# Optimization experiments

Measured on AMD Instinct MI355X. Metric: run time of the kernel, lower is better.

The kernel has to match this reference:

```python
import jax, jax.numpy as jnp
import numpy as np

NEG = -10000.0


def setup_inputs() -> dict:
    B, T, K = 512, 512, 128
    key = jax.random.key(0)
    k1, k2, k3 = jax.random.split(key, 3)
    h = jax.random.normal(k1, (B, T, K), dtype=jnp.float32)
    # transition matrix param, with the same structural masking as __init__
    trans = jax.random.normal(k2, (K, K), dtype=jnp.float32)
    PAD, START, END = 0, K - 1, K - 2  # start_tag=-1, end_tag=-2, utils.PAD=0
    trans = trans.at[START, :].set(NEG)
    trans = trans.at[:, END].set(NEG)
    trans = trans.at[:, PAD].set(NEG)
    trans = trans.at[PAD, :].set(NEG)
    trans = trans.at[PAD, END].set(0.0)
    trans = trans.at[PAD, PAD].set(0.0)
    lengths = jax.random.randint(k3, (B,), 1, T + 1, dtype=jnp.int32)
    return {"h": h, "trans": trans, "lengths": lengths}


def reference(h, trans, lengths):
    """CRF partition function (log Z) per batch element. h: [B,T,K]."""
    B, T, K = h.shape
    START, END = K - 1, K - 2
    mask = jnp.arange(T)[None, :] < lengths[:, None]  # [B, T]
    score0 = jnp.full((B, K), NEG, dtype=h.dtype).at[:, START].set(0.0)

    def step(score, xs):
        h_t, m_t = xs  # [B, K], [B]
        # score_t[b,i] = logsumexp_j(score[b,j] + trans[i,j]) + h_t[b,i]
        s = jax.nn.logsumexp(score[:, None, :] + trans[None, :, :], axis=2) + h_t
        score = jnp.where(m_t[:, None], s, score)
        return score, None

    hs = jnp.swapaxes(h, 0, 1)  # [T, B, K]
    score, _ = jax.lax.scan(step, score0, (hs, mask.T))
    return jax.nn.logsumexp(score + trans[END], axis=1)  # [B]
```

## Files before the change

### kernel.cpp

```cpp
#include <hip/hip_runtime.h>

#define T_ 512
#define K_ 128
#define L2E 1.4426950408889634f
#define LN2 0.6931471805599453f

__device__ __forceinline__ int irl(int v, int lane) {
    return __builtin_amdgcn_readlane(v, lane);
}

#if __has_builtin(__builtin_amdgcn_sdot4)
#define DOT4(a, b, c) __builtin_amdgcn_sdot4((a), (b), (c), false)
#elif __has_builtin(__builtin_amdgcn_udot4)
#define DOT4(a, b, c) ((int)__builtin_amdgcn_udot4((unsigned)(a), (unsigned)(b), (unsigned)(c), false))
#else
__device__ __forceinline__ int dot4_emu(int a, int b, int c) {
#pragma unroll
    for (int k = 0; k < 4; ++k)
        c += ((a >> (8 * k)) & 0xff) * ((b >> (8 * k)) & 0xff);
    return c;
}
#define DOT4(a, b, c) dot4_emu((a), (b), (c))
#endif

#define DPPMAX(m, ctrl)                                                     \
    m = fmaxf(m, __int_as_float(__builtin_amdgcn_update_dpp(                 \
                     0, __float_as_int(m), (ctrl), 0xf, 0xf, true)))

#define DPP_SWAP(x) __builtin_amdgcn_update_dpp(0, (x), 0xB1, 0xf, 0xf, true)

#define BODY(tt, SLOT, SNEXT)                                                \
    {                                                                        \
        const int tc = ((tt) + 4 < len) ? (tt) + 4 : len - 1;                \
        SLOT = hb[(size_t)tc * 64];                                          \
        int a0 = 0, a1 = 0, a2 = 0, a3 = 0;                                  \
        int c0 = 0, c1 = 0, c2 = 0, c3 = 0;                                  \
        _Pragma("unroll")                                                    \
        for (int d = 0; d < 32; d += 4) {                                    \
            const int u0 = irl(updw, 2 * d);                                 \
            const int u1 = irl(updw, 2 * d + 2);                             \
            const int u2 = irl(updw, 2 * d + 4);                             \
            const int u3 = irl(updw, 2 * d + 6);                             \
            a0 = DOT4(Eq0[d],     u0, a0);  c0 = DOT4(Eq1[d],     u0, c0);   \
            a1 = DOT4(Eq0[d + 1], u1, a1);  c1 = DOT4(Eq1[d + 1], u1, c1);   \
            a2 = DOT4(Eq0[d + 2], u2, a2);  c2 = DOT4(Eq1[d + 2], u2, c2);   \
            a3 = DOT4(Eq0[d + 3], u3, a3);  c3 = DOT4(Eq1[d + 3], u3, c3);   \
        }                                                                    \
        const int acc0 = (a0 + a1) + (a2 + a3);                              \
        const int acc1 = (c0 + c1) + (c2 + c3);                              \
        const float v0 = (float)acc0 * ehc0;                                 \
        const float v1 = (float)acc1 * ehc1;                                 \
        float m_ = fmaxf(v0, v1);                                            \
        DPPMAX(m_, 0x111); DPPMAX(m_, 0x112); DPPMAX(m_, 0x114);             \
        DPPMAX(m_, 0x118); DPPMAX(m_, 0x142); DPPMAX(m_, 0x143);             \
        const float mg = __int_as_float(irl(__float_as_int(m_), 63));        \
        const int   e_ = (int)(__float_as_uint(mg) >> 23) - 127;             \
        const float qs = __int_as_float((132 - e_) << 23);      \
        CMi += e_ - 5;                                                       \
        q0 = (int)fmaf(v0, qs, 0.5f);                                        \
        q1 = (int)fmaf(v1, qs, 0.5f);                                        \
        const int own16 = q0 | (q1 << 8);                                    \
        updw = own16 | (DPP_SWAP(own16) << 16);                              \
        ehc0 = exp2f(SNEXT.x * L2E) * rE0;                                   \
        ehc1 = exp2f(SNEXT.y * L2E) * rE1;                                   \
    }

__global__ __launch_bounds__(64)
__attribute__((amdgpu_waves_per_eu(1, 1)))
void crf_fwd(const float* __restrict__ h,
             const float* __restrict__ trans,
             const int* __restrict__ lengths,
             float* __restrict__ out)
{
    const int b  = blockIdx.x;
    const int l  = threadIdx.x;
    const int r0 = 2 * l, r1 = 2 * l + 1;

    const float4* ta = (const float4*)(trans + r0 * K_);
    const float4* tb = (const float4*)(trans + r1 * K_);
    float mx0 = 0.f, mx1 = 0.f;
#pragma unroll
    for (int q = 0; q < 32; ++q) {
        const float4 x = ta[q];
        mx0 = fmaxf(mx0, fmaxf(fmaxf(exp2f(x.x * L2E), exp2f(x.y * L2E)),
                               fmaxf(exp2f(x.z * L2E), exp2f(x.w * L2E))));
        const float4 y = tb[q];
        mx1 = fmaxf(mx1, fmaxf(fmaxf(exp2f(y.x * L2E), exp2f(y.y * L2E)),
                               fmaxf(exp2f(y.z * L2E), exp2f(y.w * L2E))));
    }
    mx0 = fmaxf(mx0, 1e-30f);
    mx1 = fmaxf(mx1, 1e-30f);
    const float sE0 = 127.0f / mx0, sE1 = 127.0f / mx1;
    const float rE0 = mx0 * (1.0f / 127.0f), rE1 = mx1 * (1.0f / 127.0f);

    int Eq0[32], Eq1[32];
#pragma unroll
    for (int q = 0; q < 32; ++q) {
        const float4 x = ta[q];
        const int a0 = (int)(exp2f(x.x * L2E) * sE0 + 0.5f);
        const int a1 = (int)(exp2f(x.y * L2E) * sE0 + 0.5f);
        const int a2 = (int)(exp2f(x.z * L2E) * sE0 + 0.5f);
        const int a3 = (int)(exp2f(x.w * L2E) * sE0 + 0.5f);
        Eq0[q] = a0 | (a1 << 8) | (a2 << 16) | (a3 << 24);
        const float4 y = tb[q];
        const int c0 = (int)(exp2f(y.x * L2E) * sE1 + 0.5f);
        const int c1 = (int)(exp2f(y.y * L2E) * sE1 + 0.5f);
        const int c2 = (int)(exp2f(y.z * L2E) * sE1 + 0.5f);
        const int c3 = (int)(exp2f(y.w * L2E) * sE1 + 0.5f);
        Eq1[q] = c0 | (c1 << 8) | (c2 << 16) | (c3 << 24);
    }

    const int len = lengths[b];
    const float2* hb = (const float2*)(h + (size_t)b * (T_ * K_) + r0);

    int q0 = 0, q1 = (l == 63) ? 64 : 0;
    int CMi = -6;
    int updw;
    {
        const int own16 = q0 | (q1 << 8);
        updw = own16 | (DPP_SWAP(own16) << 16);
    }

    float2 s0 = hb[0];
    float2 s1 = hb[(size_t)((1 < len) ? 1 : len - 1) * 64];
    float2 s2 = hb[(size_t)((2 < len) ? 2 : len - 1) * 64];
    float2 s3 = hb[(size_t)((3 < len) ? 3 : len - 1) * 64];
    float ehc0 = exp2f(s0.x * L2E) * rE0;
    float ehc1 = exp2f(s0.y * L2E) * rE1;

    int t = 0;
    const int nfull = len & ~3;
    for (; t < nfull; t += 4) {
        BODY(t + 0, s0, s1);
        BODY(t + 1, s1, s2);
        BODY(t + 2, s2, s3);
        BODY(t + 3, s3, s0);
    }
    if (t     < len) BODY(t,     s0, s1);
    if (t + 1 < len) BODY(t + 1, s1, s2);
    if (t + 2 < len) BODY(t + 2, s2, s3);

    const float tEa = exp2f(trans[(K_ - 2) * K_ + r0] * L2E);
    const float tEb = exp2f(trans[(K_ - 2) * K_ + r1] * L2E);
    float s = (float)q0 * tEa + (float)q1 * tEb;
#pragma unroll
    for (int off = 32; off >= 1; off >>= 1)
        s += __shfl_xor(s, off, 64);
    if (l == 0) out[b] = ((float)CMi + log2f(s)) * LN2;
}

extern "C" void kernel_launch(void* const* d_in, const int* in_sizes, int n_in,
                              void* d_out, int out_size, void* d_ws, size_t ws_size,
                              hipStream_t stream) {
    const float* h       = (const float*)d_in[0];
    const float* trans   = (const float*)d_in[1];
    const int*   lengths = (const int*)d_in[2];
    float*       out     = (float*)d_out;
    const int B = in_sizes[2];
    crf_fwd<<<B, 64, 0, stream>>>(h, trans, lengths, out);
}
```

Baseline: 178.1 us.

## Reuse previous step's quantization exponent and skip wave max reduction when in range

Each step first quantizes using the previous step's exponent and only runs the DPP cross-lane max chain and readlane when some lane overflows the 8-bit range or all values are too small. This removes a serial reduction from the per-timestep critical path on most steps. It also switches to unsigned dot4 with a 255 quantization range, which improves precision. The cost is a wave-wide vote plus a branch every step and a possible rescale path, and the first step is peeled out of the loop.

```diff
diff --git a/kernel.cpp b/kernel.cpp
--- a/kernel.cpp
+++ b/kernel.cpp
@@ -9,10 +9,12 @@
     return __builtin_amdgcn_readlane(v, lane);
 }
 
-#if __has_builtin(__builtin_amdgcn_sdot4)
+#if __has_builtin(__builtin_amdgcn_udot4)
+#define DOT4(a, b, c) ((int)__builtin_amdgcn_udot4((unsigned)(a), (unsigned)(b), (unsigned)(c), false))
+#define QMAXV 255
+#elif __has_builtin(__builtin_amdgcn_sdot4)
 #define DOT4(a, b, c) __builtin_amdgcn_sdot4((a), (b), (c), false)
-#elif __has_builtin(__builtin_amdgcn_udot4)
-#define DOT4(a, b, c) ((int)__builtin_amdgcn_udot4((unsigned)(a), (unsigned)(b), (unsigned)(c), false))
+#define QMAXV 127
 #else
 __device__ __forceinline__ int dot4_emu(int a, int b, int c) {
 #pragma unroll
@@ -21,6 +23,7 @@
     return c;
 }
 #define DOT4(a, b, c) dot4_emu((a), (b), (c))
+#define QMAXV 255
 #endif
 
 #define DPPMAX(m, ctrl)                                                     \
@@ -29,10 +32,7 @@
 
 #define DPP_SWAP(x) __builtin_amdgcn_update_dpp(0, (x), 0xB1, 0xf, 0xf, true)
 
-#define BODY(tt, SLOT, SNEXT)                                                \
-    {                                                                        \
-        const int tc = ((tt) + 4 < len) ? (tt) + 4 : len - 1;                \
-        SLOT = hb[(size_t)tc * 64];                                          \
+#define MATVEC()                                                             \
         int a0 = 0, a1 = 0, a2 = 0, a3 = 0;                                  \
         int c0 = 0, c1 = 0, c2 = 0, c3 = 0;                                  \
         _Pragma("unroll")                                                    \
@@ -48,21 +48,62 @@
         }                                                                    \
         const int acc0 = (a0 + a1) + (a2 + a3);                              \
         const int acc1 = (c0 + c1) + (c2 + c3);                              \
-        const float v0 = (float)acc0 * ehc0;                                 \
-        const float v1 = (float)acc1 * ehc1;                                 \
-        float m_ = fmaxf(v0, v1);                                            \
+        const float vpre0 = (float)acc0 * ehc0;                              \
+        const float vpre1 = (float)acc1 * ehc1;
+
+#define MAXCHAIN()                                                           \
+        float m_ = fmaxf(vpre0, vpre1);                                      \
         DPPMAX(m_, 0x111); DPPMAX(m_, 0x112); DPPMAX(m_, 0x114);             \
         DPPMAX(m_, 0x118); DPPMAX(m_, 0x142); DPPMAX(m_, 0x143);             \
-        const float mg = __int_as_float(irl(__float_as_int(m_), 63));        \
-        const int   e_ = (int)(__float_as_uint(mg) >> 23) - 127;             \
-        const float qs = __int_as_float((132 - e_) << 23);      \
+        int e_ = (int)((unsigned)irl(__float_as_int(m_), 63) >> 23) - 127;   \
+        e_ = max(e_, -20);
+
+#define PACKQ()                                                              \
+        qa = q0; qb = q1;                                                    \
+        const int own16 = q0 | (q1 << 8);                                    \
+        updw = own16 | (DPP_SWAP(own16) << 16);
+
+#define EHCNEXT(SNEXT)                                                       \
+        ehc0 = exp2f((SNEXT).x * L2E) * rE0;                                 \
+        ehc1 = exp2f((SNEXT).y * L2E) * rE1;
+
+#define BODY(tt, SLOT, SNEXT)                                                \
+    {                                                                        \
+        const int tc = ((tt) + 4 < len) ? (tt) + 4 : len - 1;                \
+        SLOT = hb[(size_t)tc * 64];                                          \
+        MATVEC();                                                            \
+        const float cnqf = __int_as_float((132 - eprev) << 23);              \
+        int q0 = (int)fminf(fmaf(vpre0, cnqf, 0.5f), 3.0e5f);                \
+        int q1 = (int)fminf(fmaf(vpre1, cnqf, 0.5f), 3.0e5f);                \
+        int eap = eprev;                                                     \
+        const int qm = max(q0, q1);                                          \
+        if (__any(qm > QMAXV) || !__any(qm >= 8)) {                          \
+            MAXCHAIN();                                                      \
+            const float cq2 = __int_as_float((132 - e_) << 23);              \
+            q0 = (int)fmaf(vpre0, cq2, 0.5f);                                \
+            q1 = (int)fmaf(vpre1, cq2, 0.5f);                                \
+            eprev = e_; eap = e_;                                            \
+        }                                                                    \
+        CMi += eap - 5;                                                      \
+        q0 = min(q0, QMAXV);  q1 = min(q1, QMAXV);                           \
+        PACKQ();                                                             \
+        EHCNEXT(SNEXT);                                                      \
+    }
+
+#define BODYX(tt, SLOT, SNEXT)                                               \
+    {                                                                        \
+        const int tc = ((tt) + 4 < len) ? (tt) + 4 : len - 1;                \
+        SLOT = hb[(size_t)tc * 64];                                          \
+        MATVEC();                                                            \
+        MAXCHAIN();                                                          \
+        const float cq2 = __int_as_float((132 - e_) << 23);                  \
+        int q0 = (int)fmaf(vpre0, cq2, 0.5f);                                \
+        int q1 = (int)fmaf(vpre1, cq2, 0.5f);                                \
+        eprev = e_;                                                          \
         CMi += e_ - 5;                                                       \
-        q0 = (int)fmaf(v0, qs, 0.5f);                                        \
-        q1 = (int)fmaf(v1, qs, 0.5f);                                        \
-        const int own16 = q0 | (q1 << 8);                                    \
-        updw = own16 | (DPP_SWAP(own16) << 16);                              \
-        ehc0 = exp2f(SNEXT.x * L2E) * rE0;                                   \
-        ehc1 = exp2f(SNEXT.y * L2E) * rE1;                                   \
+        q0 = min(q0, QMAXV);  q1 = min(q1, QMAXV);                           \
+        PACKQ();                                                             \
+        EHCNEXT(SNEXT);                                                      \
     }
 
 __global__ __launch_bounds__(64)
@@ -90,34 +131,36 @@
     }
     mx0 = fmaxf(mx0, 1e-30f);
     mx1 = fmaxf(mx1, 1e-30f);
-    const float sE0 = 127.0f / mx0, sE1 = 127.0f / mx1;
-    const float rE0 = mx0 * (1.0f / 127.0f), rE1 = mx1 * (1.0f / 127.0f);
+    const float sE0 = (float)QMAXV / mx0, sE1 = (float)QMAXV / mx1;
+    const float rE0 = mx0 * (1.0f / (float)QMAXV);
+    const float rE1 = mx1 * (1.0f / (float)QMAXV);
 
     int Eq0[32], Eq1[32];
 #pragma unroll
     for (int q = 0; q < 32; ++q) {
         const float4 x = ta[q];
-        const int a0 = (int)(exp2f(x.x * L2E) * sE0 + 0.5f);
-        const int a1 = (int)(exp2f(x.y * L2E) * sE0 + 0.5f);
-        const int a2 = (int)(exp2f(x.z * L2E) * sE0 + 0.5f);
-        const int a3 = (int)(exp2f(x.w * L2E) * sE0 + 0.5f);
-        Eq0[q] = a0 | (a1 << 8) | (a2 << 16) | (a3 << 24);
+        const int A0 = (int)(exp2f(x.x * L2E) * sE0 + 0.5f);
+        const int A1 = (int)(exp2f(x.y * L2E) * sE0 + 0.5f);
+        const int A2 = (int)(exp2f(x.z * L2E) * sE0 + 0.5f);
+        const int A3 = (int)(exp2f(x.w * L2E) * sE0 + 0.5f);
+        Eq0[q] = A0 | (A1 << 8) | (A2 << 16) | (A3 << 24);
         const float4 y = tb[q];
-        const int c0 = (int)(exp2f(y.x * L2E) * sE1 + 0.5f);
-        const int c1 = (int)(exp2f(y.y * L2E) * sE1 + 0.5f);
-        const int c2 = (int)(exp2f(y.z * L2E) * sE1 + 0.5f);
-        const int c3 = (int)(exp2f(y.w * L2E) * sE1 + 0.5f);
-        Eq1[q] = c0 | (c1 << 8) | (c2 << 16) | (c3 << 24);
+        const int C0 = (int)(exp2f(y.x * L2E) * sE1 + 0.5f);
+        const int C1 = (int)(exp2f(y.y * L2E) * sE1 + 0.5f);
+        const int C2 = (int)(exp2f(y.z * L2E) * sE1 + 0.5f);
+        const int C3 = (int)(exp2f(y.w * L2E) * sE1 + 0.5f);
+        Eq1[q] = C0 | (C1 << 8) | (C2 << 16) | (C3 << 24);
     }
 
     const int len = lengths[b];
     const float2* hb = (const float2*)(h + (size_t)b * (T_ * K_) + r0);
 
-    int q0 = 0, q1 = (l == 63) ? 64 : 0;
+    int qa = 0, qb = (l == 63) ? 64 : 0;
     int CMi = -6;
+    int eprev = 6;
     int updw;
     {
-        const int own16 = q0 | (q1 << 8);
+        const int own16 = qa | (qb << 8);
         updw = own16 | (DPP_SWAP(own16) << 16);
     }
 
@@ -128,21 +171,22 @@
     float ehc0 = exp2f(s0.x * L2E) * rE0;
     float ehc1 = exp2f(s0.y * L2E) * rE1;
 
-    int t = 0;
-    const int nfull = len & ~3;
-    for (; t < nfull; t += 4) {
-        BODY(t + 0, s0, s1);
-        BODY(t + 1, s1, s2);
-        BODY(t + 2, s2, s3);
-        BODY(t + 3, s3, s0);
-    }
-    if (t     < len) BODY(t,     s0, s1);
-    if (t + 1 < len) BODY(t + 1, s1, s2);
-    if (t + 2 < len) BODY(t + 2, s2, s3);
+    BODYX(0, s0, s1);
+
+    int t = 1;
+    for (; t + 3 < len; t += 4) {
+        BODY(t + 0, s1, s2);
+        BODY(t + 1, s2, s3);
+        BODY(t + 2, s3, s0);
+        BODY(t + 3, s0, s1);
+    }
+    if (t     < len) BODY(t,     s1, s2);
+    if (t + 1 < len) BODY(t + 1, s2, s3);
+    if (t + 2 < len) BODY(t + 2, s3, s0);
 
     const float tEa = exp2f(trans[(K_ - 2) * K_ + r0] * L2E);
     const float tEb = exp2f(trans[(K_ - 2) * K_ + r1] * L2E);
-    float s = (float)q0 * tEa + (float)q1 * tEb;
+    float s = (float)qa * tEa + (float)qb * tEb;
 #pragma unroll
     for (int off = 32; off >= 1; off >>= 1)
         s += __shfl_xor(s, off, 64);
```

Measured after the change: 205.8 us. 1.16x slower.
